# Optimization experiments

Measured on AMD Instinct MI355X. Metric: run time of the kernel, lower is better.

## Reference

```python
import jax, jax.numpy as jnp
import numpy as np

N = 50000      # nodes
E = 800000     # edges
F_NODE = 64
PE = 16
F_EDGE = 16
H = 128        # hidden_dim
L = 4          # num_layers
G = 64         # graphs in batch
NC = 10        # num_classes
BN_EPS = 1e-5


def _bn(h, g, b):
    # BatchNorm1d with batch statistics (deterministic train-style stats, no dropout)
    m = jnp.mean(h, axis=0)
    v = jnp.var(h, axis=0)
    return (h - m) * jax.lax.rsqrt(v + BN_EPS) * g + b


def setup_inputs() -> dict:
    key = jax.random.key(0)
    ks = jax.random.split(key, 16)
    p = lambda k, shape: (jax.random.normal(k, shape, jnp.float32) * 0.05)
    return dict(
        x=jax.random.normal(ks[0], (N, F_NODE), jnp.float32),
        pe=jax.random.normal(ks[1], (N, PE), jnp.float32),
        edge_index=jax.random.randint(ks[2], (2, E), 0, N),
        edge_attr=jax.random.normal(ks[3], (E, F_EDGE), jnp.float32),
        batch=jnp.sort(jax.random.randint(ks[4], (N,), 0, G)),
        W_in=p(ks[5], (F_NODE + PE, H)), b_in=jnp.zeros((H,), jnp.float32),
        We_edge=p(ks[6], (L, F_EDGE, H)), be_edge=jnp.zeros((L, H), jnp.float32),
        eps=jnp.zeros((L,), jnp.float32),
        W1_gin=p(ks[7], (L, H, 2 * H)), b1_gin=jnp.zeros((L, 2 * H), jnp.float32),
        W2_gin=p(ks[8], (L, 2 * H, H)), b2_gin=jnp.zeros((L, H), jnp.float32),
        bn1_g=jnp.ones((L, H), jnp.float32), bn1_b=jnp.zeros((L, H), jnp.float32),
        W1_ffn=p(ks[9], (L, H, 2 * H)), b1_ffn=jnp.zeros((L, 2 * H), jnp.float32),
        W2_ffn=p(ks[10], (L, 2 * H, H)), b2_ffn=jnp.zeros((L, H), jnp.float32),
        bn2_g=jnp.ones((L, H), jnp.float32), bn2_b=jnp.zeros((L, H), jnp.float32),
        W_r1=p(ks[11], (H, H)), b_r1=jnp.zeros((H,), jnp.float32),
        W_r2=p(ks[12], (H, NC)), b_r2=jnp.zeros((NC,), jnp.float32),
    )


def reference(x, pe, edge_index, edge_attr, batch,
              W_in, b_in, We_edge, be_edge, eps,
              W1_gin, b1_gin, W2_gin, b2_gin, bn1_g, bn1_b,
              W1_ffn, b1_ffn, W2_ffn, b2_ffn, bn2_g, bn2_b,
              W_r1, b_r1, W_r2, b_r2):
    src, dst = edge_index[0], edge_index[1]  # PyG: row=source j, col=target i
    # input projection on [x || pe]
    h = jax.nn.relu(jnp.concatenate([x, pe], axis=-1) @ W_in + b_in)  # [N,H]
    for l in range(L):
        # --- GINEConv: msg = relu(x_j + lin_edge(e_ij)); sum-aggregate to target
        e = edge_attr @ We_edge[l] + be_edge[l]                        # [E,H]
        msg = jax.nn.relu(h[src] + e)                                  # gather + fuse
        agg = jax.ops.segment_sum(msg, dst, num_segments=N)           # scatter-add
        z = (1.0 + eps[l]) * h + agg
        z = jax.nn.relu(z @ W1_gin[l] + b1_gin[l]) @ W2_gin[l] + b2_gin[l]
        # --- GNNPlusLayer: BN -> ReLU -> residual (identity proj, in==out)
        z = jax.nn.relu(_bn(z, bn1_g[l], bn1_b[l]))
        z = z + h
        # --- FFN (eval mode): out = lin2(relu(lin1(z))) + z, then BN
        f = jax.nn.relu(z @ W1_ffn[l] + b1_ffn[l]) @ W2_ffn[l] + b2_ffn[l]
        h = _bn(f + z, bn2_g[l], bn2_b[l])
    # --- global mean pool over graphs
    sums = jax.ops.segment_sum(h, batch, num_segments=G)               # [G,H]
    counts = jax.ops.segment_sum(jnp.ones((N,), h.dtype), batch, num_segments=G)
    hg = sums / jnp.maximum(counts, 1.0)[:, None]
    # --- readout MLP (dropout off in eval)
    return jax.nn.relu(hg @ W_r1 + b_r1) @ W_r2 + b_r2                 # [G,NC]
```

## Files before the change

kernel.cpp:

```cpp
#include <hip/hip_runtime.h>
#include <hip/hip_bf16.h>

#define NN 50000
#define NE 800000
#define FIN 80
#define H 128
#define H2 256
#define NG 64
#define NCLS 10
#define BN_EPS 1e-5f
#define NB 196
#define LDK 40

typedef __attribute__((ext_vector_type(8))) short bf16x8;
typedef __attribute__((ext_vector_type(8))) unsigned short us8;
typedef __attribute__((ext_vector_type(4))) float f32x4;

__device__ __forceinline__ unsigned short f2b(float f) {
    __hip_bfloat16 h = __float2bfloat16(f);
    return *(unsigned short*)&h;
}
__device__ __forceinline__ float b2f(unsigned short u) {
    unsigned v = (unsigned)u << 16;
    return __uint_as_float(v);
}

__global__ void wprep_all(const float* __restrict__ W1g, const float* __restrict__ W2g,
                          const float* __restrict__ W1f, const float* __restrict__ W2f,
                          unsigned short* __restrict__ wt)
{
    const int idx = blockIdx.x * 256 + threadIdx.x;
    const int m = idx >> 17;
    const int r = idx & 131071;
    const float* W;
    unsigned short* Wt;
    int K, Nn;
    if (m == 0)      { W = W1g; Wt = wt;              K = 128; Nn = 256; }
    else if (m == 1) { W = W2g; Wt = wt + 4 * 65536;  K = 256; Nn = 128; }
    else if (m == 2) { W = W1f; Wt = wt + 8 * 65536;  K = 128; Nn = 256; }
    else             { W = W2f; Wt = wt + 12 * 65536; K = 256; Nn = 128; }
    const int per = K * Nn;
    const int l = r / per;
    const int rr = r - l * per;
    const int k = rr / Nn;
    const int n = rr - k * Nn;
    const float wv = W[r];
    const unsigned short hi = f2b(wv);
    const unsigned short lo = f2b(wv - b2f(hi));
    const int KB = K >> 5;
    const int kb = k >> 5, kk = k & 31;
    unsigned short* base = Wt + (size_t)l * 2 * per;
    base[((size_t)(0 * KB + kb) * Nn + n) * 32 + kk] = hi;
    base[((size_t)(1 * KB + kb) * Nn + n) * 32 + kk] = lo;
}

template<bool ABF, bool CBF, bool ZF>
__global__ __launch_bounds__(256, 2)
void mgemm(const void* __restrict__ Ap, const unsigned short* __restrict__ Wt,
           const float* __restrict__ bias, const float* __restrict__ resid,
           void* __restrict__ Cp, int M, int K, int Nn, int relu,
           float* __restrict__ statsOut,
           const float* __restrict__ statsIn, const float* __restrict__ bng,
           const float* __restrict__ bnb, const float* __restrict__ hres,
           float* __restrict__ zout, float inv_n)
{
    __shared__ unsigned short sA[128][LDK];
    __shared__ unsigned short sB[2][128][LDK];
    __shared__ float sAB[128];
    __shared__ float sSH[128];

    const int tid = threadIdx.x;
    const int m0 = blockIdx.x * 128;
    const int n0 = blockIdx.y * 128;
    const int lane = tid & 63;
    const int w = tid >> 6;
    const int KB = K >> 5;

    if (ZF) {
        if (tid < 128) {
            const float mean = statsIn[tid] * inv_n;
            const float var = statsIn[128 + tid] * inv_n - mean * mean;
            const float a = bng[tid] * rsqrtf(var + BN_EPS);
            sAB[tid] = a;
            sSH[tid] = fmaf(-mean, a, bnb[tid]);
        }
    }

    f32x4 acc[2][8];
#pragma unroll
    for (int r = 0; r < 2; ++r)
#pragma unroll
        for (int c = 0; c < 8; ++c) acc[r][c] = (f32x4)(0.f);

    const int arow = tid >> 1;
    const int akh = (tid & 1) * 16;
    const int gm = m0 + arow;
    const int fr = lane & 15;
    const int fq = (lane >> 4) * 8;

    for (int kb = 0; kb < KB; ++kb) {
        const int k0 = kb * 32;
        __syncthreads();
        if (ABF) {
            if (gm < M) {
                const unsigned short* Ab = (const unsigned short*)Ap + (size_t)gm * K + k0 + akh;
                *(float4*)&sA[arow][akh]     = *(const float4*)Ab;
                *(float4*)&sA[arow][akh + 8] = *(const float4*)(Ab + 8);
            } else {
                *(float4*)&sA[arow][akh]     = make_float4(0.f, 0.f, 0.f, 0.f);
                *(float4*)&sA[arow][akh + 8] = make_float4(0.f, 0.f, 0.f, 0.f);
            }
        } else if (ZF) {
            if (gm < M) {
                const float* tf = (const float*)Ap + (size_t)gm * K + k0 + akh;
                const float* hf = hres + (size_t)gm * K + k0 + akh;
                float zv[16];
#pragma unroll
                for (int i = 0; i < 16; ++i) {
                    const int c = k0 + akh + i;
                    zv[i] = fmaxf(fmaf(tf[i], sAB[c], sSH[c]), 0.f) + hf[i];
                }
                if (blockIdx.y == 0) {
                    float* zo = zout + (size_t)gm * K + k0 + akh;
#pragma unroll
                    for (int i = 0; i < 16; i += 4)
                        *(float4*)(zo + i) = make_float4(zv[i], zv[i + 1], zv[i + 2], zv[i + 3]);
                }
                us8 p0, p1;
#pragma unroll
                for (int i = 0; i < 8; ++i) { p0[i] = f2b(zv[i]); p1[i] = f2b(zv[8 + i]); }
                *(us8*)&sA[arow][akh]     = p0;
                *(us8*)&sA[arow][akh + 8] = p1;
            } else {
                *(float4*)&sA[arow][akh]     = make_float4(0.f, 0.f, 0.f, 0.f);
                *(float4*)&sA[arow][akh + 8] = make_float4(0.f, 0.f, 0.f, 0.f);
            }
        } else {
            if (gm < M) {
                const float* Af = (const float*)Ap + (size_t)gm * K + k0 + akh;
                const float4 v0 = *(const float4*)(Af);
                const float4 v1 = *(const float4*)(Af + 4);
                const float4 v2 = *(const float4*)(Af + 8);
                const float4 v3 = *(const float4*)(Af + 12);
                const float vals[16] = {v0.x, v0.y, v0.z, v0.w, v1.x, v1.y, v1.z, v1.w,
                                        v2.x, v2.y, v2.z, v2.w, v3.x, v3.y, v3.z, v3.w};
                us8 p0, p1;
#pragma unroll
                for (int i = 0; i < 8; ++i) { p0[i] = f2b(vals[i]); p1[i] = f2b(vals[8 + i]); }
                *(us8*)&sA[arow][akh]     = p0;
                *(us8*)&sA[arow][akh + 8] = p1;
            } else {
                *(float4*)&sA[arow][akh]     = make_float4(0.f, 0.f, 0.f, 0.f);
                *(float4*)&sA[arow][akh + 8] = make_float4(0.f, 0.f, 0.f, 0.f);
            }
        }
#pragma unroll
        for (int p = 0; p < 2; ++p) {
            const int bn = tid >> 1;
            const int bkh = (tid & 1) * 16;
            const unsigned short* src = Wt + ((size_t)(p * KB + kb) * Nn + n0 + bn) * 32 + bkh;
            *(float4*)&sB[p][bn][bkh]     = *(const float4*)src;
            *(float4*)&sB[p][bn][bkh + 8] = *(const float4*)(src + 8);
        }
        __syncthreads();
        const bf16x8 a0 = *(const bf16x8*)&sA[w * 32 + fr][fq];
        const bf16x8 a1 = *(const bf16x8*)&sA[w * 32 + 16 + fr][fq];
#pragma unroll
        for (int c = 0; c < 8; ++c) {
            const bf16x8 bh = *(const bf16x8*)&sB[0][c * 16 + fr][fq];
            const bf16x8 bl = *(const bf16x8*)&sB[1][c * 16 + fr][fq];
            acc[0][c] = __builtin_amdgcn_mfma_f32_16x16x32_bf16(a0, bh, acc[0][c], 0, 0, 0);
            acc[0][c] = __builtin_amdgcn_mfma_f32_16x16x32_bf16(a0, bl, acc[0][c], 0, 0, 0);
            acc[1][c] = __builtin_amdgcn_mfma_f32_16x16x32_bf16(a1, bh, acc[1][c], 0, 0, 0);
            acc[1][c] = __builtin_amdgcn_mfma_f32_16x16x32_bf16(a1, bl, acc[1][c], 0, 0, 0);
        }
    }

    float s[8], q[8];
#pragma unroll
    for (int c = 0; c < 8; ++c) { s[c] = 0.f; q[c] = 0.f; }
    const int crow4 = (lane >> 4) * 4;
#pragma unroll
    for (int r = 0; r < 2; ++r) {
        const int rbase = m0 + w * 32 + r * 16 + crow4;
#pragma unroll
        for (int c = 0; c < 8; ++c) {
            const int gc = n0 + c * 16 + fr;
            const float bb = bias[gc];
#pragma unroll
            for (int reg = 0; reg < 4; ++reg) {
                const int gr = rbase + reg;
                if (gr >= M) continue;
                float o = acc[r][c][reg] + bb;
                if (resid) o += resid[(size_t)gr * Nn + gc];
                if (relu) o = fmaxf(o, 0.f);
                if (statsOut) { s[c] += o; q[c] = fmaf(o, o, q[c]); }
                if (CBF) ((unsigned short*)Cp)[(size_t)gr * Nn + gc] = f2b(o);
                else     ((float*)Cp)[(size_t)gr * Nn + gc] = o;
            }
        }
    }

    if (statsOut) {
#pragma unroll
        for (int c = 0; c < 8; ++c) {
            s[c] += __shfl_xor(s[c], 32, 64); s[c] += __shfl_xor(s[c], 16, 64);
            q[c] += __shfl_xor(q[c], 32, 64); q[c] += __shfl_xor(q[c], 16, 64);
        }
        __syncthreads();
        float* red = (float*)sA;
        if (lane < 16) {
#pragma unroll
            for (int c = 0; c < 8; ++c) {
                red[w * 128 + c * 16 + lane]       = s[c];
                red[512 + w * 128 + c * 16 + lane] = q[c];
            }
        }
        __syncthreads();
        if (tid < 128) {
            const float ss = red[tid] + red[128 + tid] + red[256 + tid] + red[384 + tid];
            const float qq = red[512 + tid] + red[640 + tid] + red[768 + tid] + red[896 + tid];
            atomicAdd(&statsOut[tid], ss);
            atomicAdd(&statsOut[128 + tid], qq);
        }
    }
}

__global__ __launch_bounds__(256, 4)
void inproj_kernel(const float* __restrict__ x, const float* __restrict__ pe,
                   const float* __restrict__ W, const float* __restrict__ bias,
                   float* __restrict__ C, unsigned short* __restrict__ Cb, int M)
{
    __shared__ float aT[16][129];
    __shared__ float wsh[16][129];

    const int tid = threadIdx.x;
    const int m0 = blockIdx.x * 128;
    const int rm = (tid >> 4) * 8;
    const int rn = (tid & 15) * 8;

    float acc[8][8];
#pragma unroll
    for (int i = 0; i < 8; ++i)
#pragma unroll
        for (int j = 0; j < 8; ++j) acc[i][j] = 0.f;

    const int lm = tid & 127;
    const int kq = (tid >> 7) * 8;
    const int wk = tid >> 4;
    const int wj = (tid & 15) * 8;

    for (int k0 = 0; k0 < FIN; k0 += 16) {
        {
            const int gm = m0 + lm;
            const int c = k0 + kq;
            if (gm < M) {
                const float* srcp = (c < 64) ? (x + (size_t)gm * 64 + c)
                                             : (pe + (size_t)gm * 16 + (c - 64));
                const float4 v0 = *(const float4*)srcp;
                const float4 v1 = *(const float4*)(srcp + 4);
                aT[kq + 0][lm] = v0.x; aT[kq + 1][lm] = v0.y;
                aT[kq + 2][lm] = v0.z; aT[kq + 3][lm] = v0.w;
                aT[kq + 4][lm] = v1.x; aT[kq + 5][lm] = v1.y;
                aT[kq + 6][lm] = v1.z; aT[kq + 7][lm] = v1.w;
            } else {
#pragma unroll
                for (int i = 0; i < 8; ++i) aT[kq + i][lm] = 0.f;
            }
        }
        {
#pragma unroll
            for (int j = 0; j < 8; ++j)
                wsh[wk][wj + j] = W[(size_t)(k0 + wk) * H + wj + j];
        }
        __syncthreads();
#pragma unroll
        for (int k = 0; k < 16; ++k) {
            const float av[8] = {aT[k][rm], aT[k][rm + 1], aT[k][rm + 2], aT[k][rm + 3],
                                 aT[k][rm + 4], aT[k][rm + 5], aT[k][rm + 6], aT[k][rm + 7]};
            const float bv[8] = {wsh[k][rn], wsh[k][rn + 1], wsh[k][rn + 2], wsh[k][rn + 3],
                                 wsh[k][rn + 4], wsh[k][rn + 5], wsh[k][rn + 6], wsh[k][rn + 7]};
#pragma unroll
            for (int i = 0; i < 8; ++i)
#pragma unroll
                for (int j = 0; j < 8; ++j)
                    acc[i][j] = fmaf(av[i], bv[j], acc[i][j]);
        }
        __syncthreads();
    }

    float bv[8];
#pragma unroll
    for (int j = 0; j < 8; ++j) bv[j] = bias[rn + j];
#pragma unroll
    for (int i = 0; i < 8; ++i) {
        const int gm = m0 + rm + i;
        if (gm >= M) continue;
        float o[8];
#pragma unroll
        for (int j = 0; j < 8; ++j) o[j] = fmaxf(acc[i][j] + bv[j], 0.f);
        *(float4*)&C[(size_t)gm * H + rn]     = make_float4(o[0], o[1], o[2], o[3]);
        *(float4*)&C[(size_t)gm * H + rn + 4] = make_float4(o[4], o[5], o[6], o[7]);
        us8 pk;
#pragma unroll
        for (int j = 0; j < 8; ++j) pk[j] = f2b(o[j]);
        *(us8*)&Cb[(size_t)gm * H + rn] = pk;
    }
}

__global__ void hist_kernel(const int* __restrict__ ei, int* __restrict__ deg)
{
    const int e = blockIdx.x * 256 + threadIdx.x;
    if (e < NE) atomicAdd(&deg[ei[NE + e]], 1);
}

__global__ void bsum_kernel(const int* __restrict__ deg, int* __restrict__ bsum)
{
    const int tid = threadIdx.x;
    const int i = blockIdx.x * 256 + tid;
    int v = (i < NN) ? deg[i] : 0;
#pragma unroll
    for (int off = 32; off > 0; off >>= 1) v += __shfl_down(v, off, 64);
    __shared__ int ws[4];
    if ((tid & 63) == 0) ws[tid >> 6] = v;
    __syncthreads();
    if (tid == 0) bsum[blockIdx.x] = ws[0] + ws[1] + ws[2] + ws[3];
}

__global__ void bscan_kernel(int* __restrict__ bsum)
{
    __shared__ int sh[256];
    const int tid = threadIdx.x;
    sh[tid] = (tid < NB) ? bsum[tid] : 0;
    __syncthreads();
    for (int off = 1; off < 256; off <<= 1) {
        const int t = (tid >= off) ? sh[tid - off] : 0;
        __syncthreads();
        sh[tid] += t;
        __syncthreads();
    }
    if (tid < NB) bsum[tid] = (tid == 0) ? 0 : sh[tid - 1];
}

__global__ void bwrite_kernel(const int* __restrict__ deg, const int* __restrict__ boff,
                              int* __restrict__ rowptr, int* __restrict__ cursor)
{
    __shared__ int sh[256];
    const int tid = threadIdx.x;
    const int i = blockIdx.x * 256 + tid;
    const int v = (i < NN) ? deg[i] : 0;
    sh[tid] = v;
    __syncthreads();
    for (int off = 1; off < 256; off <<= 1) {
        const int t = (tid >= off) ? sh[tid - off] : 0;
        __syncthreads();
        sh[tid] += t;
        __syncthreads();
    }
    if (i < NN) {
        const int pos = boff[blockIdx.x] + sh[tid] - v;
        rowptr[i] = pos;
        cursor[i] = pos;
    }
    if (blockIdx.x == 0 && tid == 0) rowptr[NN] = NE;
}

__global__ void scatter_kernel(const int* __restrict__ ei, const float* __restrict__ ea,
                               int* __restrict__ cursor, int* __restrict__ src_s,
                               float* __restrict__ ea_s)
{
    const int e = blockIdx.x * 256 + threadIdx.x;
    if (e >= NE) return;
    const int d = ei[NE + e];
    const int pos = atomicAdd(&cursor[d], 1);
    src_s[pos] = ei[e];
    const float4* sp = (const float4*)&ea[(size_t)e * 16];
    float4* dp = (float4*)&ea_s[(size_t)pos * 16];
    dp[0] = sp[0]; dp[1] = sp[1]; dp[2] = sp[2]; dp[3] = sp[3];
}

__global__ __launch_bounds__(256)
void agg_kernel(const float* __restrict__ h, const unsigned short* __restrict__ hb,
                const int* __restrict__ rowptr, const int* __restrict__ src_s,
                const float* __restrict__ ea_s, const float* __restrict__ We,
                const float* __restrict__ be, const float* __restrict__ eps, int l,
                float* __restrict__ z)
{
    const int lane = threadIdx.x & 63;
    const int w = threadIdx.x >> 6;
    const int n = blockIdx.x * 4 + w;
    if (n >= NN) return;

    float w0[16], w1[16];
#pragma unroll
    for (int k = 0; k < 16; ++k) {
        const float2 wv = *(const float2*)&We[k * H + 2 * lane];
        w0[k] = wv.x; w1[k] = wv.y;
    }
    const float2 bev = *(const float2*)&be[2 * lane];

    const int beg = __builtin_amdgcn_readfirstlane(rowptr[n]);
    const int end = __builtin_amdgcn_readfirstlane(rowptr[n + 1]);

    const float e1 = 1.0f + eps[l];
    const float2 hv0 = *(const float2*)&h[(size_t)n * H + 2 * lane];
    float acc0 = e1 * hv0.x;
    float acc1 = e1 * hv0.y;

    for (int i0 = beg; i0 < end; i0 += 8) {
        const int jn = min(8, end - i0);
        int srcs[8];
#pragma unroll
        for (int j = 0; j < 8; ++j)
            srcs[j] = src_s[(i0 + j < end) ? (i0 + j) : (end - 1)];
        unsigned hraw[8];
#pragma unroll
        for (int j = 0; j < 8; ++j)
            hraw[j] = *(const unsigned*)&hb[(size_t)srcs[j] * H + 2 * lane];
#pragma unroll
        for (int j = 0; j < 8; ++j) {
            if (j >= jn) break;
            const float* ar = ea_s + (size_t)(i0 + j) * 16;
            float s0 = bev.x, s1 = bev.y;
#pragma unroll
            for (int k = 0; k < 16; ++k) {
                const float a = ar[k];
                s0 = fmaf(a, w0[k], s0);
                s1 = fmaf(a, w1[k], s1);
            }
            const float hx = __uint_as_float(hraw[j] << 16);
            const float hy = __uint_as_float(hraw[j] & 0xffff0000u);
            acc0 += fmaxf(hx + s0, 0.f);
            acc1 += fmaxf(hy + s1, 0.f);
        }
    }
    *(float2*)&z[(size_t)n * H + 2 * lane] = make_float2(acc0, acc1);
}

__global__ void bn_apply_kernel(const float* __restrict__ u, const float* __restrict__ st,
                                const float* __restrict__ g, const float* __restrict__ b,
                                float* __restrict__ h, unsigned short* __restrict__ hb,
                                float inv_n)
{
    const int i = blockIdx.x * 256 + threadIdx.x;
    const int c = i & (H - 1);
    const float mean = st[c] * inv_n;
    const float var = st[H + c] * inv_n - mean * mean;
    const float a = g[c] * rsqrtf(var + BN_EPS);
    const float s = fmaf(-mean, a, b[c]);
    const float v = fmaf(u[i], a, s);
    h[i] = v;
    hb[i] = f2b(v);
}

__global__ void pool_kernel(const float* __restrict__ h, const int* __restrict__ batch,
                            float* __restrict__ pool, float* __restrict__ cnt, int n)
{
    const int c = threadIdx.x & (H - 1);
    const int half = threadIdx.x >> 7;
    const int r0 = blockIdx.x * 256 + half * 128;
    if (r0 >= n) return;
    const int rend = min(r0 + 128, n);
    int gprev = batch[r0];
    float acc = 0.f;
    int run = 0;
    for (int r = r0; r < rend; ++r) {
        const int g = batch[r];
        if (g != gprev) {
            atomicAdd(&pool[gprev * H + c], acc);
            if (c == 0) atomicAdd(&cnt[gprev], (float)run);
            acc = 0.f; run = 0; gprev = g;
        }
        acc += h[(size_t)r * H + c];
        run++;
    }
    atomicAdd(&pool[gprev * H + c], acc);
    if (c == 0) atomicAdd(&cnt[gprev], (float)run);
}

__global__ void readout_kernel(const float* __restrict__ pool, const float* __restrict__ cnt,
                               const float* __restrict__ Wr1, const float* __restrict__ br1,
                               const float* __restrict__ Wr2, const float* __restrict__ br2,
                               float* __restrict__ out)
{
    __shared__ float hg[H];
    __shared__ float r1[H];
    const int g = blockIdx.x;
    const int j = threadIdx.x;
    hg[j] = pool[g * H + j] / fmaxf(cnt[g], 1.0f);
    __syncthreads();
    float acc = br1[j];
    for (int k = 0; k < H; ++k) acc = fmaf(hg[k], Wr1[k * H + j], acc);
    r1[j] = fmaxf(acc, 0.f);
    __syncthreads();
    if (j < NCLS) {
        float o = br2[j];
        for (int k = 0; k < H; ++k) o = fmaf(r1[k], Wr2[k * NCLS + j], o);
        out[g * NCLS + j] = o;
    }
}

extern "C" void kernel_launch(void* const* d_in, const int* in_sizes, int n_in,
                              void* d_out, int out_size, void* d_ws, size_t ws_size,
                              hipStream_t stream)
{
    const float* x       = (const float*)d_in[0];
    const float* pe      = (const float*)d_in[1];
    const int*   ei      = (const int*)d_in[2];
    const float* ea      = (const float*)d_in[3];
    const int*   batch   = (const int*)d_in[4];
    const float* W_in    = (const float*)d_in[5];
    const float* b_in    = (const float*)d_in[6];
    const float* We_edge = (const float*)d_in[7];
    const float* be_edge = (const float*)d_in[8];
    const float* eps     = (const float*)d_in[9];
    const float* W1g     = (const float*)d_in[10];
    const float* b1g     = (const float*)d_in[11];
    const float* W2g     = (const float*)d_in[12];
    const float* b2g     = (const float*)d_in[13];
    const float* bn1g    = (const float*)d_in[14];
    const float* bn1b    = (const float*)d_in[15];
    const float* W1f     = (const float*)d_in[16];
    const float* b1f     = (const float*)d_in[17];
    const float* W2f     = (const float*)d_in[18];
    const float* b2f     = (const float*)d_in[19];
    const float* bn2g    = (const float*)d_in[20];
    const float* bn2b    = (const float*)d_in[21];
    const float* Wr1     = (const float*)d_in[22];
    const float* br1     = (const float*)d_in[23];
    const float* Wr2     = (const float*)d_in[24];
    const float* br2     = (const float*)d_in[25];
    float* out = (float*)d_out;

    const size_t NH = (size_t)NN * H;
    float* hbuf  = (float*)d_ws;
    float* zbuf  = hbuf + NH;
    float* tbuf  = zbuf + NH;
    unsigned short* z1 = (unsigned short*)(tbuf + NH);
    int*   deg   = (int*)(z1 + (size_t)NN * H2);
    float* stats = (float*)(deg + NN);
    float* pool  = stats + 2048;
    float* cnt   = pool + NG * H;
    int*   rowptr = (int*)(cnt + NG);
    int*   cursor = rowptr + NN + 1;
    int*   bsum   = cursor + NN;
    int*   src_s  = bsum + 256;
    float* ea_s   = (float*)(src_s + NE);
    unsigned short* hb = (unsigned short*)(ea_s + (size_t)NE * 16);
    unsigned short* wt = hb + NH;
    unsigned short* wt1g = wt;
    unsigned short* wt2g = wt + 4 * 65536;
    unsigned short* wt1f = wt + 8 * 65536;
    unsigned short* wt2f = wt + 12 * 65536;

    const dim3 blk(256);
    const dim3 mg1((NN + 127) / 128, 1);
    const dim3 mg2((NN + 127) / 128, 2);
    const int ew_grid = (int)(NH / 256);
    const float inv_n = 1.0f / (float)NN;
    const size_t zero_bytes = (size_t)(NN + 2048 + NG * H + NG) * 4;

    wprep_all<<<2048, blk, 0, stream>>>(W1g, W2g, W1f, W2f, wt);

    hipMemsetAsync(deg, 0, zero_bytes, stream);
    hist_kernel<<<(NE + 255) / 256, blk, 0, stream>>>(ei, deg);
    bsum_kernel<<<NB, blk, 0, stream>>>(deg, bsum);
    bscan_kernel<<<1, blk, 0, stream>>>(bsum);
    bwrite_kernel<<<NB, blk, 0, stream>>>(deg, bsum, rowptr, cursor);
    scatter_kernel<<<(NE + 255) / 256, blk, 0, stream>>>(ei, ea, cursor, src_s, ea_s);

    inproj_kernel<<<mg1, blk, 0, stream>>>(x, pe, W_in, b_in, hbuf, hb, NN);

    for (int l = 0; l < 4; ++l) {
        float* s1 = stats + (size_t)l * 512;
        float* s2 = s1 + 256;

        agg_kernel<<<(NN + 3) / 4, blk, 0, stream>>>(hbuf, hb, rowptr, src_s, ea_s,
                                                     We_edge + (size_t)l * 16 * H,
                                                     be_edge + (size_t)l * H, eps, l, zbuf);

        mgemm<false, true, false><<<mg2, blk, 0, stream>>>(
            zbuf, wt1g + (size_t)l * 65536, b1g + (size_t)l * H2, nullptr, z1,
            NN, 128, 256, 1, nullptr, nullptr, nullptr, nullptr, nullptr, nullptr, inv_n);
        mgemm<true, false, false><<<mg1, blk, 0, stream>>>(
            z1, wt2g + (size_t)l * 65536, b2g + (size_t)l * H, nullptr, tbuf,
            NN, 256, 128, 0, s1, nullptr, nullptr, nullptr, nullptr, nullptr, inv_n);

        mgemm<false, true, true><<<mg2, blk, 0, stream>>>(
            tbuf, wt1f + (size_t)l * 65536, b1f + (size_t)l * H2, nullptr, z1,
            NN, 128, 256, 1, nullptr, s1, bn1g + (size_t)l * H, bn1b + (size_t)l * H,
            hbuf, zbuf, inv_n);

        mgemm<true, false, false><<<mg1, blk, 0, stream>>>(
            z1, wt2f + (size_t)l * 65536, b2f + (size_t)l * H, zbuf, tbuf,
            NN, 256, 128, 0, s2, nullptr, nullptr, nullptr, nullptr, nullptr, inv_n);

        bn_apply_kernel<<<ew_grid, blk, 0, stream>>>(tbuf, s2, bn2g + (size_t)l * H,
                                                     bn2b + (size_t)l * H, hbuf, hb, inv_n);
    }

    pool_kernel<<<(NN + 255) / 256, blk, 0, stream>>>(hbuf, batch, pool, cnt, NN);
    readout_kernel<<<NG, H, 0, stream>>>(pool, cnt, Wr1, br1, Wr2, br2, out);
}
```

Measured before the change: 1.319 ms.

## Fuse MLP GEMM pairs with LDS-resident hidden, slab BN stats, split edge scatter

Each two-layer MLP (GIN and FFN) now runs as one kernel. The 256-wide ReLU hidden activation stays in shared memory as bf16 instead of going through a global buffer. B-operand weights are read straight from global memory rather than staged in LDS. In the FFN kernel the BN1+ReLU+residual is recomputed in the epilogue instead of storing zbuf. BatchNorm statistic atomics are spread over 8 slabs to cut contention, the edge-attribute scatter is split into an index pass and a coalesced gather, and the aggregation loop batches 16 neighbor loads instead of 8. These changes trade global memory round trips and launches for higher LDS use per block (about 78KB) and more register pressure.

After: 1.146 ms. 1.15x faster.

```diff
diff --git a/kernel.cpp b/kernel.cpp
--- a/kernel.cpp
+++ b/kernel.cpp
@@ -11,6 +11,7 @@
 #define BN_EPS 1e-5f
 #define NB 196
 #define LDK 40
+#define LDY 264
 
 typedef __attribute__((ext_vector_type(8))) short bf16x8;
 typedef __attribute__((ext_vector_type(8))) unsigned short us8;
@@ -54,175 +55,174 @@
     base[((size_t)(1 * KB + kb) * Nn + n) * 32 + kk] = lo;
 }
 
-template<bool ABF, bool CBF, bool ZF>
+template<bool ZF>
 __global__ __launch_bounds__(256, 2)
-void mgemm(const void* __restrict__ Ap, const unsigned short* __restrict__ Wt,
-           const float* __restrict__ bias, const float* __restrict__ resid,
-           void* __restrict__ Cp, int M, int K, int Nn, int relu,
-           float* __restrict__ statsOut,
-           const float* __restrict__ statsIn, const float* __restrict__ bng,
-           const float* __restrict__ bnb, const float* __restrict__ hres,
-           float* __restrict__ zout, float inv_n)
+void gemm_pair(const float* __restrict__ Ain, const float* __restrict__ hres,
+               const unsigned short* __restrict__ Wt1, const unsigned short* __restrict__ Wt2,
+               const float* __restrict__ b1, const float* __restrict__ b2,
+               const float* __restrict__ statsIn, const float* __restrict__ bng,
+               const float* __restrict__ bnb, float* __restrict__ statsOut,
+               float* __restrict__ Cout, float inv_n, int M)
 {
     __shared__ unsigned short sA[128][LDK];
-    __shared__ unsigned short sB[2][128][LDK];
+    __shared__ unsigned short sy[128][LDY];
     __shared__ float sAB[128];
     __shared__ float sSH[128];
 
     const int tid = threadIdx.x;
     const int m0 = blockIdx.x * 128;
-    const int n0 = blockIdx.y * 128;
     const int lane = tid & 63;
     const int w = tid >> 6;
-    const int KB = K >> 5;
+    const int fr = lane & 15;
+    const int fq = (lane >> 4) * 8;
+    const int crow4 = (lane >> 4) * 4;
+    const int arow = tid >> 1;
+    const int akh = (tid & 1) * 16;
+    const int gm = m0 + arow;
 
     if (ZF) {
         if (tid < 128) {
-            const float mean = statsIn[tid] * inv_n;
-            const float var = statsIn[128 + tid] * inv_n - mean * mean;
+            float su = 0.f, qu = 0.f;
+#pragma unroll
+            for (int s = 0; s < 8; ++s) {
+                su += statsIn[s * 256 + tid];
+                qu += statsIn[s * 256 + 128 + tid];
+            }
+            const float mean = su * inv_n;
+            const float var = qu * inv_n - mean * mean;
             const float a = bng[tid] * rsqrtf(var + BN_EPS);
             sAB[tid] = a;
             sSH[tid] = fmaf(-mean, a, bnb[tid]);
         }
     }
 
-    f32x4 acc[2][8];
+    f32x4 acc1[2][16];
 #pragma unroll
     for (int r = 0; r < 2; ++r)
 #pragma unroll
-        for (int c = 0; c < 8; ++c) acc[r][c] = (f32x4)(0.f);
-
-    const int arow = tid >> 1;
-    const int akh = (tid & 1) * 16;
-    const int gm = m0 + arow;
-    const int fr = lane & 15;
-    const int fq = (lane >> 4) * 8;
-
-    for (int kb = 0; kb < KB; ++kb) {
-        const int k0 = kb * 32;
-        __syncthreads();
-        if (ABF) {
-            if (gm < M) {
-                const unsigned short* Ab = (const unsigned short*)Ap + (size_t)gm * K + k0 + akh;
-                *(float4*)&sA[arow][akh]     = *(const float4*)Ab;
-                *(float4*)&sA[arow][akh + 8] = *(const float4*)(Ab + 8);
-            } else {
-                *(float4*)&sA[arow][akh]     = make_float4(0.f, 0.f, 0.f, 0.f);
-                *(float4*)&sA[arow][akh + 8] = make_float4(0.f, 0.f, 0.f, 0.f);
-            }
-        } else if (ZF) {
-            if (gm < M) {
-                const float* tf = (const float*)Ap + (size_t)gm * K + k0 + akh;
-                const float* hf = hres + (size_t)gm * K + k0 + akh;
-                float zv[16];
+        for (int c = 0; c < 16; ++c) acc1[r][c] = (f32x4)(0.f);
+
+    for (int kb = 0; kb < 4; ++kb) {
+        __syncthreads();
+        if (gm < M) {
+            const float* tf = Ain + (size_t)gm * 128 + kb * 32 + akh;
+            float zv[16];
+            if (ZF) {
+                const float* hf = hres + (size_t)gm * 128 + kb * 32 + akh;
 #pragma unroll
                 for (int i = 0; i < 16; ++i) {
-                    const int c = k0 + akh + i;
+                    const int c = kb * 32 + akh + i;
                     zv[i] = fmaxf(fmaf(tf[i], sAB[c], sSH[c]), 0.f) + hf[i];
                 }
-                if (blockIdx.y == 0) {
-                    float* zo = zout + (size_t)gm * K + k0 + akh;
-#pragma unroll
-                    for (int i = 0; i < 16; i += 4)
-                        *(float4*)(zo + i) = make_float4(zv[i], zv[i + 1], zv[i + 2], zv[i + 3]);
-                }
-                us8 p0, p1;
-#pragma unroll
-                for (int i = 0; i < 8; ++i) { p0[i] = f2b(zv[i]); p1[i] = f2b(zv[8 + i]); }
-                *(us8*)&sA[arow][akh]     = p0;
-                *(us8*)&sA[arow][akh + 8] = p1;
             } else {
-                *(float4*)&sA[arow][akh]     = make_float4(0.f, 0.f, 0.f, 0.f);
-                *(float4*)&sA[arow][akh + 8] = make_float4(0.f, 0.f, 0.f, 0.f);
+#pragma unroll
+                for (int i = 0; i < 16; ++i) zv[i] = tf[i];
             }
+            us8 p0, p1;
+#pragma unroll
+            for (int i = 0; i < 8; ++i) { p0[i] = f2b(zv[i]); p1[i] = f2b(zv[8 + i]); }
+            *(us8*)&sA[arow][akh]     = p0;
+            *(us8*)&sA[arow][akh + 8] = p1;
         } else {
-            if (gm < M) {
-                const float* Af = (const float*)Ap + (size_t)gm * K + k0 + akh;
-                const float4 v0 = *(const float4*)(Af);
-                const float4 v1 = *(const float4*)(Af + 4);
-                const float4 v2 = *(const float4*)(Af + 8);
-                const float4 v3 = *(const float4*)(Af + 12);
-                const float vals[16] = {v0.x, v0.y, v0.z, v0.w, v1.x, v1.y, v1.z, v1.w,
-                                        v2.x, v2.y, v2.z, v2.w, v3.x, v3.y, v3.z, v3.w};
-                us8 p0, p1;
-#pragma unroll
-                for (int i = 0; i < 8; ++i) { p0[i] = f2b(vals[i]); p1[i] = f2b(vals[8 + i]); }
-                *(us8*)&sA[arow][akh]     = p0;
-                *(us8*)&sA[arow][akh + 8] = p1;
-            } else {
-                *(float4*)&sA[arow][akh]     = make_float4(0.f, 0.f, 0.f, 0.f);
-                *(float4*)&sA[arow][akh + 8] = make_float4(0.f, 0.f, 0.f, 0.f);
-            }
-        }
-#pragma unroll
-        for (int p = 0; p < 2; ++p) {
-            const int bn = tid >> 1;
-            const int bkh = (tid & 1) * 16;
-            const unsigned short* src = Wt + ((size_t)(p * KB + kb) * Nn + n0 + bn) * 32 + bkh;
-            *(float4*)&sB[p][bn][bkh]     = *(const float4*)src;
-            *(float4*)&sB[p][bn][bkh + 8] = *(const float4*)(src + 8);
+            *(float4*)&sA[arow][akh]     = make_float4(0.f, 0.f, 0.f, 0.f);
+            *(float4*)&sA[arow][akh + 8] = make_float4(0.f, 0.f, 0.f, 0.f);
         }
         __syncthreads();
         const bf16x8 a0 = *(const bf16x8*)&sA[w * 32 + fr][fq];
         const bf16x8 a1 = *(const bf16x8*)&sA[w * 32 + 16 + fr][fq];
 #pragma unroll
-        for (int c = 0; c < 8; ++c) {
-            const bf16x8 bh = *(const bf16x8*)&sB[0][c * 16 + fr][fq];
-            const bf16x8 bl = *(const bf16x8*)&sB[1][c * 16 + fr][fq];
-            acc[0][c] = __builtin_amdgcn_mfma_f32_16x16x32_bf16(a0, bh, acc[0][c], 0, 0, 0);
-            acc[0][c] = __builtin_amdgcn_mfma_f32_16x16x32_bf16(a0, bl, acc[0][c], 0, 0, 0);
-            acc[1][c] = __builtin_amdgcn_mfma_f32_16x16x32_bf16(a1, bh, acc[1][c], 0, 0, 0);
-            acc[1][c] = __builtin_amdgcn_mfma_f32_16x16x32_bf16(a1, bl, acc[1][c], 0, 0, 0);
+        for (int ct = 0; ct < 16; ++ct) {
+            const bf16x8 bh = *(const bf16x8*)&Wt1[((size_t)(kb) * 256 + ct * 16 + fr) * 32 + fq];
+            const bf16x8 bl = *(const bf16x8*)&Wt1[((size_t)(4 + kb) * 256 + ct * 16 + fr) * 32 + fq];
+            acc1[0][ct] = __builtin_amdgcn_mfma_f32_16x16x32_bf16(a0, bh, acc1[0][ct], 0, 0, 0);
+            acc1[0][ct] = __builtin_amdgcn_mfma_f32_16x16x32_bf16(a0, bl, acc1[0][ct], 0, 0, 0);
+            acc1[1][ct] = __builtin_amdgcn_mfma_f32_16x16x32_bf16(a1, bh, acc1[1][ct], 0, 0, 0);
+            acc1[1][ct] = __builtin_amdgcn_mfma_f32_16x16x32_bf16(a1, bl, acc1[1][ct], 0, 0, 0);
+        }
+    }
+#pragma unroll
+    for (int ct = 0; ct < 16; ++ct) {
+        const float bb = b1[ct * 16 + fr];
+#pragma unroll
+        for (int r = 0; r < 2; ++r) {
+            const int row0 = w * 32 + r * 16 + crow4;
+#pragma unroll
+            for (int reg = 0; reg < 4; ++reg) {
+                const float o = fmaxf(acc1[r][ct][reg] + bb, 0.f);
+                sy[row0 + reg][ct * 16 + fr] = f2b(o);
+            }
+        }
+    }
+    __syncthreads();
+
+    f32x4 acc2[2][8];
+#pragma unroll
+    for (int r = 0; r < 2; ++r)
+#pragma unroll
+        for (int c = 0; c < 8; ++c) acc2[r][c] = (f32x4)(0.f);
+
+    for (int kb = 0; kb < 8; ++kb) {
+        const bf16x8 ya0 = *(const bf16x8*)&sy[w * 32 + fr][kb * 32 + fq];
+        const bf16x8 ya1 = *(const bf16x8*)&sy[w * 32 + 16 + fr][kb * 32 + fq];
+#pragma unroll
+        for (int ct = 0; ct < 8; ++ct) {
+            const bf16x8 bh = *(const bf16x8*)&Wt2[((size_t)(kb) * 128 + ct * 16 + fr) * 32 + fq];
+            const bf16x8 bl = *(const bf16x8*)&Wt2[((size_t)(8 + kb) * 128 + ct * 16 + fr) * 32 + fq];
+            acc2[0][ct] = __builtin_amdgcn_mfma_f32_16x16x32_bf16(ya0, bh, acc2[0][ct], 0, 0, 0);
+            acc2[0][ct] = __builtin_amdgcn_mfma_f32_16x16x32_bf16(ya0, bl, acc2[0][ct], 0, 0, 0);
+            acc2[1][ct] = __builtin_amdgcn_mfma_f32_16x16x32_bf16(ya1, bh, acc2[1][ct], 0, 0, 0);
+            acc2[1][ct] = __builtin_amdgcn_mfma_f32_16x16x32_bf16(ya1, bl, acc2[1][ct], 0, 0, 0);
         }
     }
 
     float s[8], q[8];
 #pragma unroll
     for (int c = 0; c < 8; ++c) { s[c] = 0.f; q[c] = 0.f; }
-    const int crow4 = (lane >> 4) * 4;
 #pragma unroll
     for (int r = 0; r < 2; ++r) {
         const int rbase = m0 + w * 32 + r * 16 + crow4;
 #pragma unroll
-        for (int c = 0; c < 8; ++c) {
-            const int gc = n0 + c * 16 + fr;
-            const float bb = bias[gc];
+        for (int ct = 0; ct < 8; ++ct) {
+            const int gc = ct * 16 + fr;
+            const float bb = b2[gc];
 #pragma unroll
             for (int reg = 0; reg < 4; ++reg) {
                 const int gr = rbase + reg;
                 if (gr >= M) continue;
-                float o = acc[r][c][reg] + bb;
-                if (resid) o += resid[(size_t)gr * Nn + gc];
-                if (relu) o = fmaxf(o, 0.f);
-                if (statsOut) { s[c] += o; q[c] = fmaf(o, o, q[c]); }
-                if (CBF) ((unsigned short*)Cp)[(size_t)gr * Nn + gc] = f2b(o);
-                else     ((float*)Cp)[(size_t)gr * Nn + gc] = o;
+                float o = acc2[r][ct][reg] + bb;
+                if (ZF) {
+                    const float tv = Ain[(size_t)gr * 128 + gc];
+                    const float hv = hres[(size_t)gr * 128 + gc];
+                    o += fmaxf(fmaf(tv, sAB[gc], sSH[gc]), 0.f) + hv;
+                }
+                s[ct] += o;
+                q[ct] = fmaf(o, o, q[ct]);
+                Cout[(size_t)gr * 128 + gc] = o;
             }
         }
     }
 
-    if (statsOut) {
+#pragma unroll
+    for (int c = 0; c < 8; ++c) {
+        s[c] += __shfl_xor(s[c], 32, 64); s[c] += __shfl_xor(s[c], 16, 64);
+        q[c] += __shfl_xor(q[c], 32, 64); q[c] += __shfl_xor(q[c], 16, 64);
+    }
+    __syncthreads();
+    float* red = (float*)sA;
+    if (lane < 16) {
 #pragma unroll
         for (int c = 0; c < 8; ++c) {
-            s[c] += __shfl_xor(s[c], 32, 64); s[c] += __shfl_xor(s[c], 16, 64);
-            q[c] += __shfl_xor(q[c], 32, 64); q[c] += __shfl_xor(q[c], 16, 64);
-        }
-        __syncthreads();
-        float* red = (float*)sA;
-        if (lane < 16) {
-#pragma unroll
-            for (int c = 0; c < 8; ++c) {
-                red[w * 128 + c * 16 + lane]       = s[c];
-                red[512 + w * 128 + c * 16 + lane] = q[c];
-            }
-        }
-        __syncthreads();
-        if (tid < 128) {
-            const float ss = red[tid] + red[128 + tid] + red[256 + tid] + red[384 + tid];
-            const float qq = red[512 + tid] + red[640 + tid] + red[768 + tid] + red[896 + tid];
-            atomicAdd(&statsOut[tid], ss);
-            atomicAdd(&statsOut[128 + tid], qq);
-        }
+            red[w * 128 + c * 16 + lane]       = s[c];
+            red[512 + w * 128 + c * 16 + lane] = q[c];
+        }
+    }
+    __syncthreads();
+    if (tid < 128) {
+        const float ss = red[tid] + red[128 + tid] + red[256 + tid] + red[384 + tid];
+        const float qq = red[512 + tid] + red[640 + tid] + red[768 + tid] + red[896 + tid];
+        float* slab = statsOut + (blockIdx.x & 7) * 256;
+        atomicAdd(&slab[tid], ss);
+        atomicAdd(&slab[128 + tid], qq);
     }
 }
 
@@ -365,18 +365,24 @@
     if (blockIdx.x == 0 && tid == 0) rowptr[NN] = NE;
 }
 
-__global__ void scatter_kernel(const int* __restrict__ ei, const float* __restrict__ ea,
-                               int* __restrict__ cursor, int* __restrict__ src_s,
-                               float* __restrict__ ea_s)
+__global__ void scat_idx(const int* __restrict__ ei, int* __restrict__ cursor,
+                         int* __restrict__ src_s, int* __restrict__ perm)
 {
     const int e = blockIdx.x * 256 + threadIdx.x;
     if (e >= NE) return;
-    const int d = ei[NE + e];
-    const int pos = atomicAdd(&cursor[d], 1);
+    const int pos = atomicAdd(&cursor[ei[NE + e]], 1);
     src_s[pos] = ei[e];
-    const float4* sp = (const float4*)&ea[(size_t)e * 16];
-    float4* dp = (float4*)&ea_s[(size_t)pos * 16];
-    dp[0] = sp[0]; dp[1] = sp[1]; dp[2] = sp[2]; dp[3] = sp[3];
+    perm[pos] = e;
+}
+
+__global__ void gather_ea(const float* __restrict__ ea, const int* __restrict__ perm,
+                          float* __restrict__ ea_s)
+{
+    const int idx = blockIdx.x * 256 + threadIdx.x;
+    const int pos = idx >> 2;
+    const int qd = idx & 3;
+    const int e = perm[pos];
+    *(float4*)&ea_s[(size_t)pos * 16 + qd * 4] = *(const float4*)&ea[(size_t)e * 16 + qd * 4];
 }
 
 __global__ __launch_bounds__(256)
@@ -407,18 +413,18 @@
     float acc0 = e1 * hv0.x;
     float acc1 = e1 * hv0.y;
 
-    for (int i0 = beg; i0 < end; i0 += 8) {
-        const int jn = min(8, end - i0);
-        int srcs[8];
-#pragma unroll
-        for (int j = 0; j < 8; ++j)
+    for (int i0 = beg; i0 < end; i0 += 16) {
+        const int jn = min(16, end - i0);
+        int srcs[16];
+#pragma unroll
+        for (int j = 0; j < 16; ++j)
             srcs[j] = src_s[(i0 + j < end) ? (i0 + j) : (end - 1)];
-        unsigned hraw[8];
-#pragma unroll
-        for (int j = 0; j < 8; ++j)
+        unsigned hraw[16];
+#pragma unroll
+        for (int j = 0; j < 16; ++j)
             hraw[j] = *(const unsigned*)&hb[(size_t)srcs[j] * H + 2 * lane];
 #pragma unroll
-        for (int j = 0; j < 8; ++j) {
+        for (int j = 0; j < 16; ++j) {
             if (j >= jn) break;
             const float* ar = ea_s + (size_t)(i0 + j) * 16;
             float s0 = bev.x, s1 = bev.y;
@@ -444,11 +450,14 @@
 {
     const int i = blockIdx.x * 256 + threadIdx.x;
     const int c = i & (H - 1);
-    const float mean = st[c] * inv_n;
-    const float var = st[H + c] * inv_n - mean * mean;
+    float su = 0.f, qu = 0.f;
+#pragma unroll
+    for (int s = 0; s < 8; ++s) { su += st[s * 256 + c]; qu += st[s * 256 + 128 + c]; }
+    const float mean = su * inv_n;
+    const float var = qu * inv_n - mean * mean;
     const float a = g[c] * rsqrtf(var + BN_EPS);
-    const float s = fmaf(-mean, a, b[c]);
-    const float v = fmaf(u[i], a, s);
+    const float sh = fmaf(-mean, a, b[c]);
+    const float v = fmaf(u[i], a, sh);
     h[i] = v;
     hb[i] = f2b(v);
 }
@@ -536,10 +545,10 @@
     float* hbuf  = (float*)d_ws;
     float* zbuf  = hbuf + NH;
     float* tbuf  = zbuf + NH;
-    unsigned short* z1 = (unsigned short*)(tbuf + NH);
-    int*   deg   = (int*)(z1 + (size_t)NN * H2);
+    int*   perm  = (int*)(tbuf + NH);
+    int*   deg   = perm + NE;
     float* stats = (float*)(deg + NN);
-    float* pool  = stats + 2048;
+    float* pool  = stats + 16384;
     float* cnt   = pool + NG * H;
     int*   rowptr = (int*)(cnt + NG);
     int*   cursor = rowptr + NN + 1;
@@ -555,10 +564,9 @@
 
     const dim3 blk(256);
     const dim3 mg1((NN + 127) / 128, 1);
-    const dim3 mg2((NN + 127) / 128, 2);
     const int ew_grid = (int)(NH / 256);
     const float inv_n = 1.0f / (float)NN;
-    const size_t zero_bytes = (size_t)(NN + 2048 + NG * H + NG) * 4;
+    const size_t zero_bytes = (size_t)(NN + 16384 + NG * H + NG) * 4;
 
     wprep_all<<<2048, blk, 0, stream>>>(W1g, W2g, W1f, W2f, wt);
 
@@ -567,33 +575,28 @@
     bsum_kernel<<<NB, blk, 0, stream>>>(deg, bsum);
     bscan_kernel<<<1, blk, 0, stream>>>(bsum);
     bwrite_kernel<<<NB, blk, 0, stream>>>(deg, bsum, rowptr, cursor);
-    scatter_kernel<<<(NE + 255) / 256, blk, 0, stream>>>(ei, ea, cursor, src_s, ea_s);
+    scat_idx<<<(NE + 255) / 256, blk, 0, stream>>>(ei, cursor, src_s, perm);
+    gather_ea<<<(NE * 4) / 256, blk, 0, stream>>>(ea, perm, ea_s);
 
     inproj_kernel<<<mg1, blk, 0, stream>>>(x, pe, W_in, b_in, hbuf, hb, NN);
 
     for (int l = 0; l < 4; ++l) {
-        float* s1 = stats + (size_t)l * 512;
-        float* s2 = s1 + 256;
+        float* s1 = stats + (size_t)l * 4096;
+        float* s2 = s1 + 2048;
 
         agg_kernel<<<(NN + 3) / 4, blk, 0, stream>>>(hbuf, hb, rowptr, src_s, ea_s,
                                                      We_edge + (size_t)l * 16 * H,
                                                      be_edge + (size_t)l * H, eps, l, zbuf);
 
-        mgemm<false, true, false><<<mg2, blk, 0, stream>>>(
-            zbuf, wt1g + (size_t)l * 65536, b1g + (size_t)l * H2, nullptr, z1,
-            NN, 128, 256, 1, nullptr, nullptr, nullptr, nullptr, nullptr, nullptr, inv_n);
-        mgemm<true, false, false><<<mg1, blk, 0, stream>>>(
-            z1, wt2g + (size_t)l * 65536, b2g + (size_t)l * H, nullptr, tbuf,
-            NN, 256, 128, 0, s1, nullptr, nullptr, nullptr, nullptr, nullptr, inv_n);
-
-        mgemm<false, true, true><<<mg2, blk, 0, stream>>>(
-            tbuf, wt1f + (size_t)l * 65536, b1f + (size_t)l * H2, nullptr, z1,
-            NN, 128, 256, 1, nullptr, s1, bn1g + (size_t)l * H, bn1b + (size_t)l * H,
-            hbuf, zbuf, inv_n);
-
-        mgemm<true, false, false><<<mg1, blk, 0, stream>>>(
-            z1, wt2f + (size_t)l * 65536, b2f + (size_t)l * H, zbuf, tbuf,
-            NN, 256, 128, 0, s2, nullptr, nullptr, nullptr, nullptr, nullptr, inv_n);
+        gemm_pair<false><<<mg1, blk, 0, stream>>>(
+            zbuf, nullptr, wt1g + (size_t)l * 65536, wt2g + (size_t)l * 65536,
+            b1g + (size_t)l * H2, b2g + (size_t)l * H,
+            nullptr, nullptr, nullptr, s1, tbuf, inv_n, NN);
+
+        gemm_pair<true><<<mg1, blk, 0, stream>>>(
+            tbuf, hbuf, wt1f + (size_t)l * 65536, wt2f + (size_t)l * 65536,
+            b1f + (size_t)l * H2, b2f + (size_t)l * H,
+            s1, bn1g + (size_t)l * H, bn1b + (size_t)l * H, s2, tbuf, inv_n, NN);
 
         bn_apply_kernel<<<ew_grid, blk, 0, stream>>>(tbuf, s2, bn2g + (size_t)l * H,
                                                      bn2b + (size_t)l * H, hbuf, hb, inv_n);
```
